# Optimization experiments

Hardware: AMD Instinct MI355X
Metric: run time of the kernel (lower is better)

## Reference

```python
import jax, jax.numpy as jnp
import numpy as np

NHEAD = 8
ROUTING_STEPS = 2
TEMP = 1.0
ROPE_THETA = 10000.0


def rmsnorm(x, w, eps=1e-6):
    return x * jax.lax.rsqrt(jnp.mean(x * x, axis=-1, keepdims=True) + eps) * w


def rope_cos_sin(seq_len, head_dim, theta):
    inv = 1.0 / (theta ** (jnp.arange(0, head_dim, 2, dtype=jnp.float32) / head_dim))
    freqs = jnp.outer(jnp.arange(seq_len, dtype=jnp.float32), inv)  # [S, hd/2]
    return jnp.cos(freqs), jnp.sin(freqs)


def apply_rope(x, cos, sin):
    # x: [B,H,S,hd]; cos/sin: [S, hd/2]
    x1, x2 = x[..., 0::2], x[..., 1::2]
    c, s = cos[None, None], sin[None, None]
    r1 = x1 * c - x2 * s
    r2 = x1 * s + x2 * c
    return jnp.stack([r1, r2], axis=-1).reshape(x.shape)


def cube_forward(x, wq, wk, wv, wo, w1, w2, g1, g2, cos, sin):
    # Per-sample gathered expert weights: wq.. [B,D,D], w1 [B,D,F], w2 [B,F,D]
    B, S, D = x.shape
    H = NHEAD
    hd = D // H
    xn = rmsnorm(x, g1[:, None, :])
    q = jnp.einsum('bsd,bde->bse', xn, wq).reshape(B, S, H, hd).transpose(0, 2, 1, 3)
    k = jnp.einsum('bsd,bde->bse', xn, wk).reshape(B, S, H, hd).transpose(0, 2, 1, 3)
    v = jnp.einsum('bsd,bde->bse', xn, wv).reshape(B, S, H, hd).transpose(0, 2, 1, 3)
    q = apply_rope(q, cos, sin)
    k = apply_rope(k, cos, sin)
    scores = jnp.einsum('bhqd,bhkd->bhqk', q, k) / jnp.sqrt(jnp.float32(hd))
    causal = jnp.tril(jnp.ones((S, S), dtype=bool))
    scores = jnp.where(causal, scores, jnp.float32(-1e30))
    att = jax.nn.softmax(scores, axis=-1)
    o = jnp.einsum('bhqk,bhkd->bhqd', att, v).transpose(0, 2, 1, 3).reshape(B, S, D)
    x = x + jnp.einsum('bsd,bde->bse', o, wo)
    hn = rmsnorm(x, g2[:, None, :])
    ff = jax.nn.silu(jnp.einsum('bsd,bdf->bsf', hn, w1))
    return x + jnp.einsum('bsf,bfd->bsd', ff, w2)


def reference(input_ids, start_cubes, emb, Wq, Wk, Wv, Wo, W1, W2, n1, n2, gate_w, final_norm_w, fc_out_w):
    B, S = input_ids.shape
    D = emb.shape[1]
    C = Wq.shape[0]
    x = emb[input_ids] * jnp.sqrt(jnp.float32(D))
    cos, sin = rope_cos_sin(S, D // NHEAD, ROPE_THETA)
    # deterministic ring graph: neighbors of cube i are (i+1)%C and (i+2)%C
    ar = jnp.arange(C)
    adj = jnp.zeros((C, C), dtype=bool).at[ar, (ar + 1) % C].set(True).at[ar, (ar + 2) % C].set(True)
    cur = start_cubes
    acc_probs = jnp.zeros(C + 1, dtype=jnp.float32)
    acc_lb = jnp.float32(0.0)
    for _ in range(ROUTING_STEPS):
        x = cube_forward(x, Wq[cur], Wk[cur], Wv[cur], Wo[cur], W1[cur], W2[cur], n1[cur], n2[cur], cos, sin)
        pooled = x.mean(axis=1)                        # [B, D]
        scores = pooled @ gate_w                       # [B, C+1]
        probs = jax.nn.softmax(scores / TEMP, axis=-1)
        acc_probs = acc_probs + probs.sum(axis=0)
        avg = probs.mean(axis=0)
        acc_lb = acc_lb + (C + 1) * jnp.sum(avg * avg)
        masked = jnp.where(adj[cur], scores[:, :C], jnp.float32(-1e30))
        cur = jnp.argmax(masked, axis=-1)
    logits = jnp.einsum('bsd,dv->bsv', rmsnorm(x, final_norm_w), fc_out_w)
    avg_probs = acc_probs / jnp.float32(ROUTING_STEPS * B)
    aux_variance_loss = jnp.var(avg_probs)
    aux_lb_loss = acc_lb / jnp.float32(ROUTING_STEPS)
    return logits, aux_variance_loss, aux_lb_loss


def setup_inputs() -> dict:
    key = jax.random.key(0)
    ks = jax.random.split(key, 16)
    V, D, F, C, B, S = 32000, 512, 2048, 4, 2, 256
    w = 0.02
    return {
        'input_ids': jax.random.randint(ks[0], (B, S), 0, V),
        'start_cubes': jax.random.randint(ks[1], (B,), 0, C),
        'emb': jax.random.normal(ks[2], (V, D), jnp.float32) * w,
        'Wq': jax.random.normal(ks[3], (C, D, D), jnp.float32) * w,
        'Wk': jax.random.normal(ks[4], (C, D, D), jnp.float32) * w,
        'Wv': jax.random.normal(ks[5], (C, D, D), jnp.float32) * w,
        'Wo': jax.random.normal(ks[6], (C, D, D), jnp.float32) * w,
        'W1': jax.random.normal(ks[7], (C, D, F), jnp.float32) * w,
        'W2': jax.random.normal(ks[8], (C, F, D), jnp.float32) * w,
        'n1': jnp.ones((C, D), jnp.float32),
        'n2': jnp.ones((C, D), jnp.float32),
        'gate_w': jax.random.normal(ks[9], (D, C + 1), jnp.float32) * w,
        'final_norm_w': jnp.ones((D,), jnp.float32),
        'fc_out_w': jax.random.normal(ks[10], (D, V), jnp.float32) * w,
    }
```

## Files before the change

### kernel.cpp

```cpp
#include <hip/hip_runtime.h>
#include <hip/hip_bf16.h>

#define BB 2
#define SS 256
#define DDIM 512
#define HH 8
#define HDIM 64
#define FDIM 2048
#define CC 4
#define VV 32000
#define NTOK (BB*SS)
#define PCHUNK 16

typedef __hip_bfloat16 bf16;
typedef __attribute__((ext_vector_type(8))) short short8;
typedef __attribute__((ext_vector_type(4))) short short4v;
typedef __attribute__((ext_vector_type(4))) float floatx4;

__device__ __forceinline__ int get_mode(const unsigned* __restrict__ probe) {
    return (probe[0] == 0x3F800000u) ? 0 : 1;
}
__device__ __forceinline__ float ldw(const void* __restrict__ p, long i, int mode) {
    if (mode == 0) return ((const float*)p)[i];
    return __bfloat162float(((const bf16*)p)[i]);
}
__device__ __forceinline__ void stf(void* __restrict__ p, long i, float v, int mode) {
    if (mode == 0) ((float*)p)[i] = v;
    else ((bf16*)p)[i] = __float2bfloat16(v);
}

__device__ __forceinline__ void gload16(const void* g, void* l) {
    __builtin_amdgcn_global_load_lds(
        (const __attribute__((address_space(1))) unsigned int*)g,
        (__attribute__((address_space(3))) unsigned int*)l, 16, 0, 0);
}

__global__ void init_kernel(const int* __restrict__ ids,
                            const int* __restrict__ start_cubes,
                            const void* __restrict__ emb,
                            float* __restrict__ x,
                            float* __restrict__ acc_probs,
                            float* __restrict__ acc_lb,
                            int* __restrict__ cur,
                            const unsigned* __restrict__ probe) {
    int mode = get_mode(probe);
    int gid = blockIdx.x * blockDim.x + threadIdx.x;
    if (gid < NTOK * DDIM) {
        int tok = gid / DDIM, d = gid % DDIM;
        x[gid] = ldw(emb, (long)ids[tok] * DDIM + d, mode) * 22.627416997969522f;
    }
    if (gid < CC + 1) acc_probs[gid] = 0.f;
    if (gid == CC + 1) *acc_lb = 0.f;
    if (gid < BB) cur[gid] = start_cubes[gid];
}

__global__ void rmsnorm_kernel(const float* __restrict__ in,
                               void* __restrict__ out, int obf,
                               const void* __restrict__ gamma,
                               const int* __restrict__ cur,
                               float* __restrict__ zbuf, int zn,
                               const unsigned* __restrict__ probe) {
    int mode = get_mode(probe);
    int tok = blockIdx.x;
    int b = tok / SS;
    long goff = cur ? (long)cur[b] * DDIM : 0;
    if (zbuf) {
        int gtid = blockIdx.x * blockDim.x + threadIdx.x;
        int gstride = gridDim.x * blockDim.x;
        for (int i = gtid; i < zn; i += gstride) zbuf[i] = 0.f;
    }
    __shared__ float red[256];
    int t = threadIdx.x;
    float x0 = in[(long)tok * DDIM + t];
    float x1 = in[(long)tok * DDIM + t + 256];
    red[t] = x0 * x0 + x1 * x1;
    __syncthreads();
    for (int s = 128; s > 0; s >>= 1) {
        if (t < s) red[t] += red[t + s];
        __syncthreads();
    }
    float scale = rsqrtf(red[0] / DDIM + 1e-6f);
    float v0 = x0 * scale * ldw(gamma, goff + t, mode);
    float v1 = x1 * scale * ldw(gamma, goff + t + 256, mode);
    if (obf) {
        ((bf16*)out)[(long)tok * DDIM + t]       = __float2bfloat16(v0);
        ((bf16*)out)[(long)tok * DDIM + t + 256] = __float2bfloat16(v1);
    } else {
        ((float*)out)[(long)tok * DDIM + t]       = v0;
        ((float*)out)[(long)tok * DDIM + t + 256] = v1;
    }
}

__global__ void silu_kernel(const float* __restrict__ in,
                            ushort* __restrict__ out, int n) {
    int i4 = (blockIdx.x * blockDim.x + threadIdx.x) * 4;
    if (i4 >= n) return;
    float4 v = *(const float4*)&in[i4];
    float a = v.x / (1.f + expf(-v.x));
    float b = v.y / (1.f + expf(-v.y));
    float c = v.z / (1.f + expf(-v.z));
    float d = v.w / (1.f + expf(-v.w));
    bf16 t0 = __float2bfloat16(a), t1 = __float2bfloat16(b);
    bf16 t2 = __float2bfloat16(c), t3 = __float2bfloat16(d);
    short4v o;
    o[0] = *(short*)&t0; o[1] = *(short*)&t1;
    o[2] = *(short*)&t2; o[3] = *(short*)&t3;
    *(short4v*)&out[i4] = o;
}

__global__ void transpose_kernel(const void* __restrict__ in, bf16* __restrict__ out,
                                 int K, int N, long ims, long oms,
                                 const unsigned* __restrict__ probe) {
    int mode = get_mode(probe);
    __shared__ float tile[32][33];
    int mat = blockIdx.z;
    int n0 = blockIdx.x * 32, k0 = blockIdx.y * 32;
    int tx = threadIdx.x, ty = threadIdx.y;
#pragma unroll
    for (int i = 0; i < 4; i++)
        tile[ty + i * 8][tx] = ldw(in, (long)mat * ims + (long)(k0 + ty + i * 8) * N + (n0 + tx), mode);
    __syncthreads();
#pragma unroll
    for (int i = 0; i < 4; i++)
        out[(long)mat * oms + (long)(n0 + ty + i * 8) * K + (k0 + tx)] =
            __float2bfloat16(tile[tx][ty + i * 8]);
}

__global__ __launch_bounds__(256)
void gemm_mfma(const ushort* __restrict__ A,
               const ushort* __restrict__ WtB,
               const int* __restrict__ cur, long wcube, long wz,
               int K, int N,
               const float* __restrict__ res,
               void* __restrict__ out, long ozstride,
               int omode, int ACT, int nsplit, int swz,
               const unsigned* __restrict__ probe) {
    int mode = get_mode(probe);
    __shared__ __align__(16) ushort sA[128 * 32];
    __shared__ __align__(16) ushort sB[128 * 32];
    int tid = threadIdx.x;
    int mi = blockIdx.y, ni = blockIdx.x;
    if (swz) {
        int nb = gridDim.x, mb = gridDim.y;
        int lin = blockIdx.x + blockIdx.y * nb;
        int nwg = nb * mb;
        int q = nwg >> 3;
        int xcd = lin & 7, pos = lin >> 3;
        int nid = xcd * q + pos;
        mi = nid % mb;
        ni = nid / mb;
    }
    int m0 = mi * 128;
    int n0 = ni * 128;
    int z  = blockIdx.z / nsplit;
    int ks = blockIdx.z % nsplit;
    int Kc = K / nsplit;
    int kbeg = ks * Kc, kend = kbeg + Kc;
    const ushort* Wt = WtB + (long)z * wz + (cur ? (long)cur[m0 / SS] * wcube : 0);
    floatx4 acc[4][4];
#pragma unroll
    for (int i = 0; i < 4; i++)
#pragma unroll
        for (int j = 0; j < 4; j++)
#pragma unroll
            for (int r = 0; r < 4; r++) acc[i][j][r] = 0.f;
    int w = tid >> 6, lane = tid & 63;
    int wm = (w & 1) * 64, wn = (w >> 1) * 64;
    int lr = lane & 15, quad = lane >> 4;

    for (int k0 = kbeg; k0 < kend; k0 += 32) {
        __syncthreads();
#pragma unroll
        for (int i = 0; i < 2; i++) {
            int g = tid + i * 256;
            int r = g >> 2, c8 = (g & 3) * 8;
            gload16(&A[(long)(m0 + r) * K + k0 + c8],  &sA[g * 8]);
            gload16(&Wt[(long)(n0 + r) * K + k0 + c8], &sB[g * 8]);
        }
        __syncthreads();
        short8 af[4], bfr[4];
#pragma unroll
        for (int i = 0; i < 4; i++) {
            af[i]  = *(const short8*)&sA[(wm + i * 16 + lr) * 32 + quad * 8];
            bfr[i] = *(const short8*)&sB[(wn + i * 16 + lr) * 32 + quad * 8];
        }
#pragma unroll
        for (int mm = 0; mm < 4; mm++)
#pragma unroll
            for (int nn = 0; nn < 4; nn++)
                acc[mm][nn] = __builtin_amdgcn_mfma_f32_16x16x32_bf16(af[mm], bfr[nn], acc[mm][nn], 0, 0, 0);
    }
#pragma unroll
    for (int mm = 0; mm < 4; mm++)
#pragma unroll
        for (int nn = 0; nn < 4; nn++) {
            int col = n0 + wn + nn * 16 + lr;
#pragma unroll
            for (int r = 0; r < 4; r++) {
                int row = m0 + wm + mm * 16 + quad * 4 + r;
                float v = acc[mm][nn][r];
                long oi = (long)z * ozstride + (long)row * N + col;
                if (omode == 3) {
                    atomicAdd((float*)out + oi, v);
                } else {
                    if (ACT == 1) v = v / (1.f + expf(-v));
                    if (res) v += res[(long)row * N + col];
                    if (omode == 0)      ((float*)out)[oi] = v;
                    else if (omode == 1) ((bf16*)out)[oi] = __float2bfloat16(v);
                    else                 stf(out, oi, v, mode);
                }
            }
        }
}

__global__ void rope_kernel(float* __restrict__ q, float* __restrict__ k) {
    int gid = blockIdx.x * blockDim.x + threadIdx.x;
    if (gid >= NTOK * HH * (HDIM / 2)) return;
    int j = gid % (HDIM / 2);
    int rest = gid / (HDIM / 2);
    int h = rest % HH;
    int tok = rest / HH;
    int s = tok % SS;
    float inv = expf(-(float)j * (logf(10000.f) / 32.f));
    float ang = (float)s * inv;
    float c = cosf(ang), sn = sinf(ang);
    long base = (long)tok * DDIM + h * HDIM + 2 * j;
    float q1 = q[base], q2 = q[base + 1];
    q[base]     = q1 * c - q2 * sn;
    q[base + 1] = q1 * sn + q2 * c;
    float k1 = k[base], k2 = k[base + 1];
    k[base]     = k1 * c - k2 * sn;
    k[base + 1] = k1 * sn + k2 * c;
}

__global__ void attn_kernel(const float* __restrict__ q,
                            const float* __restrict__ k,
                            const float* __restrict__ v,
                            void* __restrict__ o, int obf) {
    int blk = blockIdx.x;
    int qr = blk % SS;
    int h = (blk / SS) % HH;
    int b = blk / (SS * HH);
    int t = threadIdx.x;
    __shared__ float sc[256];
    __shared__ float red[256];
    __shared__ float qs[HDIM];
    long qbase = ((long)(b * SS + qr)) * DDIM + h * HDIM;
    if (t < HDIM) qs[t] = q[qbase + t];
    __syncthreads();
    float s = -1e30f;
    if (t <= qr) {
        long kbase = ((long)(b * SS + t)) * DDIM + h * HDIM;
        float acc = 0.f;
#pragma unroll
        for (int i = 0; i < HDIM; i++) acc += qs[i] * k[kbase + i];
        s = acc * 0.125f;
    }
    sc[t] = s;
    red[t] = s;
    __syncthreads();
    for (int st = 128; st > 0; st >>= 1) {
        if (t < st) red[t] = fmaxf(red[t], red[t + st]);
        __syncthreads();
    }
    float m = red[0];
    __syncthreads();
    float e = (t <= qr) ? expf(sc[t] - m) : 0.f;
    sc[t] = e;
    red[t] = e;
    __syncthreads();
    for (int st = 128; st > 0; st >>= 1) {
        if (t < st) red[t] += red[t + st];
        __syncthreads();
    }
    float invsum = 1.f / red[0];
    __syncthreads();
    int g = t >> 6, d = t & 63;
    float pacc = 0.f;
    for (int kk = g; kk <= qr; kk += 4)
        pacc += sc[kk] * v[((long)(b * SS + kk)) * DDIM + h * HDIM + d];
    red[t] = pacc;
    __syncthreads();
    if (t < HDIM) {
        float vv = (red[t] + red[t + 64] + red[t + 128] + red[t + 192]) * invsum;
        if (obf) ((bf16*)o)[qbase + t] = __float2bfloat16(vv);
        else     ((float*)o)[qbase + t] = vv;
    }
}

__global__ void pool_partial_kernel(const float* __restrict__ x,
                                    float* __restrict__ partial) {
    int blk = blockIdx.x;
    int b = blk / (SS / PCHUNK);
    int c = blk % (SS / PCHUNK);
    int t = threadIdx.x;
    float acc = 0.f;
    long base = ((long)b * SS + c * PCHUNK) * DDIM + t;
#pragma unroll
    for (int i = 0; i < PCHUNK; i++) acc += x[base + (long)i * DDIM];
    partial[(long)blk * DDIM + t] = acc;
}

__global__ void routing_kernel(const float* __restrict__ partial,
                               const void* __restrict__ gate_w,
                               float* __restrict__ acc_probs,
                               float* __restrict__ acc_lb,
                               int* __restrict__ cur,
                               int final_step,
                               void* __restrict__ d_out,
                               const unsigned* __restrict__ probe) {
    int mode = get_mode(probe);
    __shared__ float pooled[BB][DDIM];
    __shared__ float scores[BB][CC + 1];
    int t = threadIdx.x;
#pragma unroll
    for (int b = 0; b < BB; b++) {
        float acc = 0.f;
#pragma unroll
        for (int c = 0; c < SS / PCHUNK; c++)
            acc += partial[((long)b * (SS / PCHUNK) + c) * DDIM + t];
        pooled[b][t] = acc / (float)SS;
    }
    __syncthreads();
    if (t < BB * (CC + 1)) {
        int b = t / (CC + 1), c = t % (CC + 1);
        float acc = 0.f;
        for (int d = 0; d < DDIM; d++)
            acc += pooled[b][d] * ldw(gate_w, (long)d * (CC + 1) + c, mode);
        scores[b][c] = acc;
    }
    __syncthreads();
    if (t == 0) {
        float probs[BB][CC + 1];
        for (int b = 0; b < BB; b++) {
            float m = -1e30f;
            for (int c = 0; c <= CC; c++) m = fmaxf(m, scores[b][c]);
            float sum = 0.f;
            for (int c = 0; c <= CC; c++) { probs[b][c] = expf(scores[b][c] - m); sum += probs[b][c]; }
            for (int c = 0; c <= CC; c++) probs[b][c] /= sum;
        }
        float lb = 0.f;
        for (int c = 0; c <= CC; c++) {
            float sumb = 0.f;
            for (int b = 0; b < BB; b++) sumb += probs[b][c];
            acc_probs[c] += sumb;
            float avg = sumb / (float)BB;
            lb += avg * avg;
        }
        *acc_lb += (float)(CC + 1) * lb;
        for (int b = 0; b < BB; b++) {
            int cu = cur[b];
            int a1 = (cu + 1) % CC, a2 = (cu + 2) % CC;
            float best = -1e38f; int bi = 0;
            for (int c = 0; c < CC; c++) {
                float vv = (c == a1 || c == a2) ? scores[b][c] : -1e30f;
                if (vv > best) { best = vv; bi = c; }
            }
            cur[b] = bi;
        }
        if (final_step) {
            float ap[CC + 1], mean = 0.f;
            for (int c = 0; c <= CC; c++) { ap[c] = acc_probs[c] / (2.f * BB); mean += ap[c]; }
            mean /= (float)(CC + 1);
            float var = 0.f;
            for (int c = 0; c <= CC; c++) { float d = ap[c] - mean; var += d * d; }
            var /= (float)(CC + 1);
            stf(d_out, (long)NTOK * VV + 0, var, mode);
            stf(d_out, (long)NTOK * VV + 1, (*acc_lb) / 2.f, mode);
        }
    }
}

template <int TM, int ACT, bool OUT_DYN>
__global__ void gemm_kernel(const float* __restrict__ A,
                            const void* __restrict__ Wbase,
                            const int* __restrict__ cur, long wstride,
                            int K, int N,
                            const float* __restrict__ res,
                            void* __restrict__ out,
                            const unsigned* __restrict__ probe) {
    int mode = get_mode(probe);
    extern __shared__ float sA[];
    int row0 = blockIdx.y * TM;
    long woff = cur ? (long)cur[row0 / SS] * wstride : 0;
    int t = threadIdx.x;
    for (int i = t; i < TM * K; i += 256)
        sA[i] = A[(long)(row0 + i / K) * K + (i % K)];
    __syncthreads();
    int n = blockIdx.x * 256 + t;
    float acc[TM];
#pragma unroll
    for (int r = 0; r < TM; r++) acc[r] = 0.f;
    for (int k = 0; k < K; k++) {
        float w = ldw(Wbase, woff + (long)k * N + n, mode);
#pragma unroll
        for (int r = 0; r < TM; r++) acc[r] += sA[r * K + k] * w;
    }
#pragma unroll
    for (int r = 0; r < TM; r++) {
        float v = acc[r];
        if (ACT == 1) v = v / (1.f + expf(-v));
        if (res) v += res[(long)(row0 + r) * N + n];
        long oi = (long)(row0 + r) * N + n;
        if constexpr (OUT_DYN) stf(out, oi, v, mode);
        else                   ((float*)out)[oi] = v;
    }
}

__global__ void routing_kernel_fb(const float* __restrict__ x,
                                  const void* __restrict__ gate_w,
                                  float* __restrict__ acc_probs,
                                  float* __restrict__ acc_lb,
                                  int* __restrict__ cur,
                                  int final_step,
                                  void* __restrict__ d_out,
                                  const unsigned* __restrict__ probe) {
    int mode = get_mode(probe);
    __shared__ float pooled[BB][DDIM];
    __shared__ float scores[BB][CC + 1];
    int t = threadIdx.x;
    for (int b = 0; b < BB; b++) {
        float acc = 0.f;
        for (int s = 0; s < SS; s++) acc += x[((long)(b * SS + s)) * DDIM + t];
        pooled[b][t] = acc / (float)SS;
    }
    __syncthreads();
    if (t < BB * (CC + 1)) {
        int b = t / (CC + 1), c = t % (CC + 1);
        float acc = 0.f;
        for (int d = 0; d < DDIM; d++)
            acc += pooled[b][d] * ldw(gate_w, (long)d * (CC + 1) + c, mode);
        scores[b][c] = acc;
    }
    __syncthreads();
    if (t == 0) {
        float probs[BB][CC + 1];
        for (int b = 0; b < BB; b++) {
            float m = -1e30f;
            for (int c = 0; c <= CC; c++) m = fmaxf(m, scores[b][c]);
            float sum = 0.f;
            for (int c = 0; c <= CC; c++) { probs[b][c] = expf(scores[b][c] - m); sum += probs[b][c]; }
            for (int c = 0; c <= CC; c++) probs[b][c] /= sum;
        }
        float lb = 0.f;
        for (int c = 0; c <= CC; c++) {
            float sumb = 0.f;
            for (int b = 0; b < BB; b++) sumb += probs[b][c];
            acc_probs[c] += sumb;
            float avg = sumb / (float)BB;
            lb += avg * avg;
        }
        *acc_lb += (float)(CC + 1) * lb;
        for (int b = 0; b < BB; b++) {
            int cu = cur[b];
            int a1 = (cu + 1) % CC, a2 = (cu + 2) % CC;
            float best = -1e38f; int bi = 0;
            for (int c = 0; c < CC; c++) {
                float vv = (c == a1 || c == a2) ? scores[b][c] : -1e30f;
                if (vv > best) { best = vv; bi = c; }
            }
            cur[b] = bi;
        }
        if (final_step) {
            float ap[CC + 1], mean = 0.f;
            for (int c = 0; c <= CC; c++) { ap[c] = acc_probs[c] / (2.f * BB); mean += ap[c]; }
            mean /= (float)(CC + 1);
            float var = 0.f;
            for (int c = 0; c <= CC; c++) { float d = ap[c] - mean; var += d * d; }
            var /= (float)(CC + 1);
            stf(d_out, (long)NTOK * VV + 0, var, mode);
            stf(d_out, (long)NTOK * VV + 1, (*acc_lb) / 2.f, mode);
        }
    }
}

extern "C" void kernel_launch(void* const* d_in, const int* in_sizes, int n_in,
                              void* d_out, int out_size, void* d_ws, size_t ws_size,
                              hipStream_t stream) {
    const int*  ids   = (const int*)d_in[0];
    const int*  start = (const int*)d_in[1];
    const void* emb   = d_in[2];
    const void* Wq    = d_in[3];
    const void* Wk    = d_in[4];
    const void* Wv    = d_in[5];
    const void* Wo    = d_in[6];
    const void* W1    = d_in[7];
    const void* W2    = d_in[8];
    const void* n1    = d_in[9];
    const void* n2    = d_in[10];
    const void* gate  = d_in[11];
    const void* fnorm = d_in[12];
    const void* fcw   = d_in[13];
    const unsigned* probe = (const unsigned*)d_in[9];

    char* base = (char*)d_ws;
    size_t off = 0;
    auto alloc = [&](size_t bytes) { size_t p = off; off = (off + bytes + 255) & ~(size_t)255; return p; };
    size_t x_o    = alloc((size_t)NTOK * DDIM * 4);
    size_t qkv_o  = alloc((size_t)3 * NTOK * DDIM * 4);
    size_t xn_o   = alloc((size_t)NTOK * DDIM * 2);
    size_t ob_o   = alloc((size_t)NTOK * DDIM * 2);
    size_t ff_o   = alloc((size_t)NTOK * FDIM * 2);
    size_t ffp_o  = alloc((size_t)NTOK * FDIM * 4);
    size_t acc_o  = alloc(256);
    size_t part_o = alloc((size_t)BB * (SS / PCHUNK) * DDIM * 4);
    size_t qkvT_o = alloc((size_t)3 * CC * DDIM * DDIM * 2);
    size_t WoT_o  = alloc((size_t)CC * DDIM * DDIM * 2);
    size_t W1T_o  = alloc((size_t)CC * DDIM * FDIM * 2);
    size_t W2T_o  = alloc((size_t)CC * FDIM * DDIM * 2);
    size_t fcwT_o = alloc((size_t)DDIM * VV * 2);
    bool big = ws_size >= off;

    if (big) {
        float* x    = (float*)(base + x_o);
        float* qkv  = (float*)(base + qkv_o);
        float* q = qkv, *k = qkv + NTOK * DDIM, *v = qkv + 2 * NTOK * DDIM;
        bf16*  xn   = (bf16*)(base + xn_o);
        bf16*  ob   = (bf16*)(base + ob_o);
        bf16*  ff   = (bf16*)(base + ff_o);
        float* ffp  = (float*)(base + ffp_o);
        float* acc_probs = (float*)(base + acc_o);
        float* acc_lb = acc_probs + 8;
        int*   cur = (int*)(acc_lb + 8);
        float* partial = (float*)(base + part_o);
        bf16* qkvT = (bf16*)(base + qkvT_o);
        bf16* WoT  = (bf16*)(base + WoT_o);
        bf16* W1T  = (bf16*)(base + W1T_o);
        bf16* W2T  = (bf16*)(base + W2T_o);
        bf16* fcwT = (bf16*)(base + fcwT_o);

        dim3 tb(32, 8);
        transpose_kernel<<<dim3(16, 16, CC), tb, 0, stream>>>(Wq, qkvT,                 DDIM, DDIM, (long)DDIM*DDIM, (long)DDIM*DDIM, probe);
        transpose_kernel<<<dim3(16, 16, CC), tb, 0, stream>>>(Wk, qkvT +   CC*DDIM*DDIM, DDIM, DDIM, (long)DDIM*DDIM, (long)DDIM*DDIM, probe);
        transpose_kernel<<<dim3(16, 16, CC), tb, 0, stream>>>(Wv, qkvT + 2*CC*DDIM*DDIM, DDIM, DDIM, (long)DDIM*DDIM, (long)DDIM*DDIM, probe);
        transpose_kernel<<<dim3(16, 16, CC), tb, 0, stream>>>(Wo, WoT,  DDIM, DDIM, (long)DDIM*DDIM, (long)DDIM*DDIM, probe);
        transpose_kernel<<<dim3(64, 16, CC), tb, 0, stream>>>(W1, W1T,  DDIM, FDIM, (long)DDIM*FDIM, (long)FDIM*DDIM, probe);
        transpose_kernel<<<dim3(16, 64, CC), tb, 0, stream>>>(W2, W2T,  FDIM, DDIM, (long)FDIM*DDIM, (long)DDIM*FDIM, probe);
        transpose_kernel<<<dim3(1000, 16, 1), tb, 0, stream>>>(fcw, fcwT, DDIM, VV, 0, 0, probe);

        init_kernel<<<(NTOK * DDIM + 255) / 256, 256, 0, stream>>>(
            ids, start, emb, x, acc_probs, acc_lb, cur, probe);

        const long DD2 = (long)DDIM * DDIM;
        const int QS = 4;
        const int OS = 4;
        const int F1S = 4;
        const int F2S = 8;
        for (int step = 0; step < 2; step++) {
            rmsnorm_kernel<<<NTOK, 256, 0, stream>>>(x, xn, 1, n1, cur,
                                                     qkv, 3 * NTOK * DDIM, probe);
            gemm_mfma<<<dim3(DDIM/128, NTOK/128, 3*QS), 256, 0, stream>>>(
                (const ushort*)xn, (const ushort*)qkvT, cur, DD2, (long)CC*DD2,
                DDIM, DDIM, nullptr, qkv, (long)NTOK*DDIM, 3, 0, QS, 0, probe);
            rope_kernel<<<(NTOK * HH * (HDIM / 2) + 255) / 256, 256, 0, stream>>>(q, k);
            attn_kernel<<<BB * HH * SS, 256, 0, stream>>>(q, k, v, ob, 1);
            gemm_mfma<<<dim3(DDIM/128, NTOK/128, OS), 256, 0, stream>>>(
                (const ushort*)ob, (const ushort*)WoT, cur, DD2, 0,
                DDIM, DDIM, nullptr, x, 0, 3, 0, OS, 0, probe);
            rmsnorm_kernel<<<NTOK, 256, 0, stream>>>(x, xn, 1, n2, cur,
                                                     ffp, NTOK * FDIM, probe);
            gemm_mfma<<<dim3(FDIM/128, NTOK/128, F1S), 256, 0, stream>>>(
                (const ushort*)xn, (const ushort*)W1T, cur, (long)FDIM*DDIM, 0,
                DDIM, FDIM, nullptr, ffp, 0, 3, 0, F1S, 0, probe);
            silu_kernel<<<(NTOK * FDIM / 4 + 255) / 256, 256, 0, stream>>>(
                ffp, (ushort*)ff, NTOK * FDIM);
            gemm_mfma<<<dim3(DDIM/128, NTOK/128, F2S), 256, 0, stream>>>(
                (const ushort*)ff, (const ushort*)W2T, cur, (long)DDIM*FDIM, 0,
                FDIM, DDIM, nullptr, x, 0, 3, 0, F2S, 0, probe);
            pool_partial_kernel<<<BB * (SS / PCHUNK), 512, 0, stream>>>(x, partial);
            routing_kernel<<<1, 512, 0, stream>>>(
                partial, gate, acc_probs, acc_lb, cur, step == 1, d_out, probe);
        }
        rmsnorm_kernel<<<NTOK, 256, 0, stream>>>(x, xn, 1, fnorm, nullptr,
                                                 nullptr, 0, probe);
        gemm_mfma<<<dim3(VV/128, NTOK/128, 1), 256, 0, stream>>>(
            (const ushort*)xn, (const ushort*)fcwT, nullptr, 0, 0,
            DDIM, VV, nullptr, d_out, 0, 2, 0, 1, 1, probe);
        return;
    }

    float* ws = (float*)d_ws;
    float* x  = ws;
    float* xn = x  + NTOK * DDIM;
    float* q  = xn + NTOK * DDIM;
    float* k  = q  + NTOK * DDIM;
    float* v  = k  + NTOK * DDIM;
    float* o  = v  + NTOK * DDIM;
    float* ff = o  + NTOK * DDIM;
    float* acc_probs = ff + NTOK * FDIM;
    float* acc_lb    = acc_probs + 8;
    int*   cur       = (int*)(acc_lb + 8);
    const long DD2 = (long)DDIM * DDIM;

    init_kernel<<<(NTOK * DDIM + 255) / 256, 256, 0, stream>>>(
        ids, start, emb, x, acc_probs, acc_lb, cur, probe);
    for (int step = 0; step < 2; step++) {
        rmsnorm_kernel<<<NTOK, 256, 0, stream>>>(x, xn, 0, n1, cur, nullptr, 0, probe);
        dim3 gdd(DDIM / 256, NTOK / 16);
        size_t smem16 = 16 * DDIM * sizeof(float);
        gemm_kernel<16, 0, false><<<gdd, 256, smem16, stream>>>(
            xn, Wq, cur, DD2, DDIM, DDIM, nullptr, q, probe);
        gemm_kernel<16, 0, false><<<gdd, 256, smem16, stream>>>(
            xn, Wk, cur, DD2, DDIM, DDIM, nullptr, k, probe);
        gemm_kernel<16, 0, false><<<gdd, 256, smem16, stream>>>(
            xn, Wv, cur, DD2, DDIM, DDIM, nullptr, v, probe);
        rope_kernel<<<(NTOK * HH * (HDIM / 2) + 255) / 256, 256, 0, stream>>>(q, k);
        attn_kernel<<<BB * HH * SS, 256, 0, stream>>>(q, k, v, o, 0);
        gemm_kernel<16, 0, false><<<gdd, 256, smem16, stream>>>(
            o, Wo, cur, DD2, DDIM, DDIM, x, x, probe);
        rmsnorm_kernel<<<NTOK, 256, 0, stream>>>(x, xn, 0, n2, cur, nullptr, 0, probe);
        dim3 gdf(FDIM / 256, NTOK / 16);
        gemm_kernel<16, 1, false><<<gdf, 256, smem16, stream>>>(
            xn, W1, cur, (long)DDIM * FDIM, DDIM, FDIM, nullptr, ff, probe);
        dim3 gfd(DDIM / 256, NTOK / 4);
        size_t smem4f = 4 * FDIM * sizeof(float);
        gemm_kernel<4, 0, false><<<gfd, 256, smem4f, stream>>>(
            ff, W2, cur, (long)FDIM * DDIM, FDIM, DDIM, x, x, probe);
        routing_kernel_fb<<<1, 512, 0, stream>>>(
            x, gate, acc_probs, acc_lb, cur, step == 1, d_out, probe);
    }
    rmsnorm_kernel<<<NTOK, 256, 0, stream>>>(x, xn, 0, fnorm, nullptr, nullptr, 0, probe);
    dim3 gv(VV / 256, NTOK / 16);
    size_t smem16 = 16 * DDIM * sizeof(float);
    gemm_kernel<16, 0, true><<<gv, 256, smem16, stream>>>(
        xn, fcw, nullptr, 0, DDIM, VV, nullptr, d_out, probe);
}
```

Before: 596.6 us.

## Double-buffer GEMM LDS tiles with XOR swizzle and vectorize attention QK dot

```diff
diff --git a/kernel.cpp b/kernel.cpp
--- a/kernel.cpp
+++ b/kernel.cpp
@@ -136,8 +136,8 @@
                int omode, int ACT, int nsplit, int swz,
                const unsigned* __restrict__ probe) {
     int mode = get_mode(probe);
-    __shared__ __align__(16) ushort sA[128 * 32];
-    __shared__ __align__(16) ushort sB[128 * 32];
+    __shared__ __align__(16) ushort sA[2][128 * 32];
+    __shared__ __align__(16) ushort sB[2][128 * 32];
     int tid = threadIdx.x;
     int mi = blockIdx.y, ni = blockIdx.x;
     if (swz) {
@@ -155,7 +155,7 @@
     int z  = blockIdx.z / nsplit;
     int ks = blockIdx.z % nsplit;
     int Kc = K / nsplit;
-    int kbeg = ks * Kc, kend = kbeg + Kc;
+    int kbeg = ks * Kc;
     const ushort* Wt = WtB + (long)z * wz + (cur ? (long)cur[m0 / SS] * wcube : 0);
     floatx4 acc[4][4];
 #pragma unroll
@@ -168,27 +168,47 @@
     int wm = (w & 1) * 64, wn = (w >> 1) * 64;
     int lr = lane & 15, quad = lane >> 4;
 
-    for (int k0 = kbeg; k0 < kend; k0 += 32) {
-        __syncthreads();
+    auto stage = [&](int buf, int k0) {
 #pragma unroll
         for (int i = 0; i < 2; i++) {
-            int g = tid + i * 256;
-            int r = g >> 2, c8 = (g & 3) * 8;
-            gload16(&A[(long)(m0 + r) * K + k0 + c8],  &sA[g * 8]);
-            gload16(&Wt[(long)(n0 + r) * K + k0 + c8], &sB[g * 8]);
-        }
-        __syncthreads();
+            int g  = tid + i * 256;
+            int gs = g ^ ((g >> 3) & 7);
+            int rs = gs >> 2, cs = (gs & 3) * 8;
+            gload16(&A[(long)(m0 + rs) * K + k0 + cs],  &sA[buf][g * 8]);
+            gload16(&Wt[(long)(n0 + rs) * K + k0 + cs], &sB[buf][g * 8]);
+        }
+    };
+
+    int nsteps = Kc >> 5;
+    stage(0, kbeg);
+    for (int j = 0; j < nsteps; ++j) {
+        int cu = j & 1;
+        if (j + 1 < nsteps) {
+            stage(cu ^ 1, kbeg + ((j + 1) << 5));
+            asm volatile("s_waitcnt vmcnt(4)" ::: "memory");
+        } else {
+            asm volatile("s_waitcnt vmcnt(0)" ::: "memory");
+        }
+        __builtin_amdgcn_sched_barrier(0);
+        __builtin_amdgcn_s_barrier();
         short8 af[4], bfr[4];
 #pragma unroll
         for (int i = 0; i < 4; i++) {
-            af[i]  = *(const short8*)&sA[(wm + i * 16 + lr) * 32 + quad * 8];
-            bfr[i] = *(const short8*)&sB[(wn + i * 16 + lr) * 32 + quad * 8];
+            int oA = (wm + i * 16 + lr) * 4 + quad;
+            int sa = oA ^ ((oA >> 3) & 7);
+            af[i]  = *(const short8*)&sA[cu][sa * 8];
+            int oB = (wn + i * 16 + lr) * 4 + quad;
+            int sb = oB ^ ((oB >> 3) & 7);
+            bfr[i] = *(const short8*)&sB[cu][sb * 8];
         }
 #pragma unroll
         for (int mm = 0; mm < 4; mm++)
 #pragma unroll
             for (int nn = 0; nn < 4; nn++)
                 acc[mm][nn] = __builtin_amdgcn_mfma_f32_16x16x32_bf16(af[mm], bfr[nn], acc[mm][nn], 0, 0, 0);
+        asm volatile("s_waitcnt lgkmcnt(0)" ::: "memory");
+        __builtin_amdgcn_sched_barrier(0);
+        __builtin_amdgcn_s_barrier();
     }
 #pragma unroll
     for (int mm = 0; mm < 4; mm++)
@@ -244,16 +264,21 @@
     int t = threadIdx.x;
     __shared__ float sc[256];
     __shared__ float red[256];
-    __shared__ float qs[HDIM];
+    __shared__ __align__(16) float qs[HDIM];
     long qbase = ((long)(b * SS + qr)) * DDIM + h * HDIM;
     if (t < HDIM) qs[t] = q[qbase + t];
     __syncthreads();
     float s = -1e30f;
     if (t <= qr) {
         long kbase = ((long)(b * SS + t)) * DDIM + h * HDIM;
+        const float4* k4 = (const float4*)&k[kbase];
+        const float4* q4 = (const float4*)qs;
         float acc = 0.f;
 #pragma unroll
-        for (int i = 0; i < HDIM; i++) acc += qs[i] * k[kbase + i];
+        for (int i = 0; i < HDIM / 4; i++) {
+            float4 a = q4[i], bv = k4[i];
+            acc += a.x * bv.x + a.y * bv.y + a.z * bv.z + a.w * bv.w;
+        }
         s = acc * 0.125f;
     }
     sc[t] = s;
```

Measured after the change: 594.2 us. About the same (-0.4%).
